# Kernel tuning notes

Measured on AMD Instinct MI355X. Metric: run time of the kernel, lower is better.

The kernel has to match this reference:

```python
import jax, jax.numpy as jnp
import numpy as np
import math

# Zero-indexed Fano plane lines: {i, i+1, i+3} mod 7
FANO_LINES = np.array([[0,1,3],[1,2,4],[2,3,5],[3,4,6],[4,5,0],[5,6,1],[6,0,2]])
WINDOW = 16  # local window hardcoded in create_expanded_mask

HIDDEN = 896
HEADS = 7
HEAD_DIM = HIDDEN // HEADS  # 128
B, T = 4, 2048


def fano_expanded_mask(T, causal):
    # line membership per head: [7, T] -> True where (j % 7) in line
    jm = np.arange(T) % 7
    line_hit = np.zeros((7, T), dtype=bool)
    for h in range(7):
        line_hit[h] = np.isin(jm, FANO_LINES[h])
    line_hit = jnp.asarray(line_hit)
    i = jnp.arange(T)[:, None]
    j = jnp.arange(T)[None, :]
    if causal:
        causal_m = j <= i                      # [T, T]
        local = (j >= i - WINDOW) & (j <= i)   # causal local window [i-16, i]
        mask = (line_hit[:, None, :] & causal_m[None]) | local[None]
    else:
        local = (j >= i - WINDOW) & (j <= i + WINDOW)
        mask = line_hit[:, None, :] | local[None]
    return mask  # [7, T, T], True = attend


def setup_inputs() -> dict:
    key = jax.random.key(0)
    kx, kq, kk, kv, ko = jax.random.split(key, 5)
    s = 1.0 / math.sqrt(HIDDEN)
    return {
        "x": jax.random.normal(kx, (B, T, HIDDEN), dtype=jnp.float32),
        "Wq": jax.random.normal(kq, (HEADS, HIDDEN, HEAD_DIM), dtype=jnp.float32) * s,
        "Wk": jax.random.normal(kk, (HEADS, HIDDEN, HEAD_DIM), dtype=jnp.float32) * s,
        "Wv": jax.random.normal(kv, (HEADS, HIDDEN, HEAD_DIM), dtype=jnp.float32) * s,
        "Wo": jax.random.normal(ko, (HIDDEN, HIDDEN), dtype=jnp.float32) * s,
        "is_causal": 1,
    }


def reference(x, Wq, Wk, Wv, Wo, is_causal):
    Bx, Tx, H = x.shape
    d = Wq.shape[-1]
    scale = 1.0 / math.sqrt(d)
    # per-head projections (no bias): [7, B, T, d]
    q = jnp.einsum('bth,nhd->nbtd', x, Wq)
    k = jnp.einsum('bth,nhd->nbtd', x, Wk)
    v = jnp.einsum('bth,nhd->nbtd', x, Wv)
    mask = fano_expanded_mask(Tx, bool(is_causal))        # [7, T, T]
    attn = jnp.einsum('nbtd,nbsd->nbts', q, k) * scale    # [7, B, T, T]
    attn = jnp.where(mask[:, None], attn, -jnp.inf)
    attn = jax.nn.softmax(attn, axis=-1)                  # every row has j=i valid
    out = jnp.einsum('nbts,nbsd->nbtd', attn, v)          # [7, B, T, d]
    combined = out.transpose(1, 2, 0, 3).reshape(Bx, Tx, H)  # concat heads
    return combined @ Wo.T
```

## Files before the change

### kernel.cpp

```cpp
#include <hip/hip_runtime.h>
#include <hip/hip_bf16.h>

#define HIDDEN 896
#define HEADS 7
#define HDIM 128
#define BB 4
#define TT 2048
#define MTOT (BB*TT)

#define SCP 896

typedef short bf16x8 __attribute__((ext_vector_type(8)));
typedef float f32x4 __attribute__((ext_vector_type(4)));

__device__ __forceinline__ short f2bf(float f) {
    union { float f; unsigned u; } v; v.f = f;
    unsigned r = (v.u + 0x7FFF + ((v.u >> 16) & 1)) >> 16;
    return (short)r;
}

__device__ __forceinline__ void gll16(const short* g, short* l) {
    __builtin_amdgcn_global_load_lds(
        (const __attribute__((address_space(1))) unsigned int*)g,
        (__attribute__((address_space(3))) unsigned int*)l, 16, 0, 0);
}

__device__ __forceinline__ unsigned linemask(int h) {
    return ((0x0Bu << h) | (0x0Bu >> (7 - h))) & 0x7Fu;
}
__device__ __forceinline__ int linecnt(unsigned m, int X) {
    return (X / 7) * 3 + __popc(m & ((1u << (X % 7)) - 1u));
}

#define NB_CASTX (MTOT * HIDDEN / 1024)
#define NB_CASTWO (HIDDEN * HIDDEN / 1024)
#define NB_TRANS (28 * 4 * 21)
__global__ __launch_bounds__(256) void prep_fused(
    const float* __restrict__ x, const float* __restrict__ Wo,
    const float* __restrict__ Wq, const float* __restrict__ Wk,
    const float* __restrict__ Wv,
    short* __restrict__ xb, short* __restrict__ Wob, short* __restrict__ Wt)
{
    __shared__ float tile[32][33];
    const int bid = blockIdx.x;
    if (bid < NB_CASTX) {
        int base = (bid * 256 + threadIdx.x) * 4;
        float4 v = *(const float4*)(x + base);
        short4 o;
        o.x = f2bf(v.x); o.y = f2bf(v.y); o.z = f2bf(v.z); o.w = f2bf(v.w);
        *(short4*)(xb + base) = o;
    } else if (bid < NB_CASTX + NB_CASTWO) {
        int base = ((bid - NB_CASTX) * 256 + threadIdx.x) * 4;
        float4 v = *(const float4*)(Wo + base);
        short4 o;
        o.x = f2bf(v.x); o.y = f2bf(v.y); o.z = f2bf(v.z); o.w = f2bf(v.w);
        *(short4*)(Wob + base) = o;
    } else {
        int t = bid - NB_CASTX - NB_CASTWO;
        const int z = t / 112;
        const int rem = t % 112;
        const int bx = rem % 28, by = rem / 28;
        const int type = z / 7, head = z % 7;
        const float* src = (type == 0 ? Wq : (type == 1 ? Wk : Wv)) + head * (HIDDEN * HDIM);
        short* dst = Wt + (size_t)z * (HDIM * HIDDEN);
        const int r0 = bx * 32, c0 = by * 32;
        const int tx = threadIdx.x & 31, ty = threadIdx.x >> 5;
        for (int i = 0; i < 4; i++)
            tile[ty * 4 + i][tx] = src[(r0 + ty * 4 + i) * HDIM + c0 + tx];
        __syncthreads();
        for (int i = 0; i < 4; i++)
            dst[(c0 + ty * 4 + i) * HIDDEN + r0 + tx] = f2bf(tile[tx][ty * 4 + i]);
    }
}

__global__ __launch_bounds__(256) void qkv_gemm(
    const short* __restrict__ xb, const short* __restrict__ Wt,
    short* __restrict__ Q, short* __restrict__ Kk, short* __restrict__ Vt)
{
    __shared__ short Ash[3 * 128 * 32];
    __shared__ short Bsh[3 * 128 * 32];
    const int orig = blockIdx.x;
    const int sblk = (orig & 7) * 168 + (orig >> 3);
    const int z = sblk % 21;
    const int m0 = (sblk / 21) * 128;
    const int head = z % 7, type = z / 7;
    const short* Wz = Wt + (size_t)z * (HDIM * HIDDEN);

    const int tid = threadIdx.x;
    const int wave = tid >> 6, lane = tid & 63;
    const int quad = lane >> 4, l16 = lane & 15;
    const int wm = (wave >> 1) * 64, wn = (wave & 1) * 64;

    f32x4 acc[4][4] = {};

    const int r0 = tid >> 2, cc0 = (tid & 3) * 8;
    const int r1 = r0 + 64;
    const short* asrc0 = xb + (size_t)(m0 + r0) * HIDDEN + cc0;
    const short* asrc1 = xb + (size_t)(m0 + r1) * HIDDEN + cc0;
    const short* bsrc0 = Wz + (size_t)r0 * HIDDEN + cc0;
    const short* bsrc1 = Wz + (size_t)r1 * HIDDEN + cc0;

    auto STAGE = [&](int kt, int sel) {
        const int ko = kt * 32;
        short* ab = Ash + sel * 4096;
        short* bb = Bsh + sel * 4096;
        gll16(asrc0 + ko, ab + wave * 512);
        gll16(asrc1 + ko, ab + 2048 + wave * 512);
        gll16(bsrc0 + ko, bb + wave * 512);
        gll16(bsrc1 + ko, bb + 2048 + wave * 512);
    };

    STAGE(0, 0);
    const int NT = HIDDEN / 32;
    for (int t = 0; t < NT; t++) {
        const int sel = t % 3;
        if (t + 1 < NT) {
            STAGE(t + 1, (t + 1) % 3);
            asm volatile("s_waitcnt vmcnt(4)" ::: "memory");
        } else {
            asm volatile("s_waitcnt vmcnt(0)" ::: "memory");
        }
        __builtin_amdgcn_s_barrier();
        __builtin_amdgcn_sched_barrier(0);
        const short* ab = Ash + sel * 4096;
        const short* bb = Bsh + sel * 4096;
        bf16x8 af[4], bfr[4];
        for (int mi = 0; mi < 4; mi++)
            af[mi] = *(const bf16x8*)(ab + (wm + mi * 16 + l16) * 32 + quad * 8);
        for (int ni = 0; ni < 4; ni++)
            bfr[ni] = *(const bf16x8*)(bb + (wn + ni * 16 + l16) * 32 + quad * 8);
        for (int mi = 0; mi < 4; mi++)
            for (int ni = 0; ni < 4; ni++)
                acc[mi][ni] = __builtin_amdgcn_mfma_f32_16x16x32_bf16(af[mi], bfr[ni], acc[mi][ni], 0, 0, 0);
    }

    const size_t base = (size_t)head * (MTOT * HDIM);
    if (type == 0) {
        const float qs = 0.08838834764831845f * 1.4426950408889634f;
        for (int mi = 0; mi < 4; mi++)
            for (int ni = 0; ni < 4; ni++)
                for (int r = 0; r < 4; r++) {
                    int m = m0 + wm + mi * 16 + quad * 4 + r;
                    int n = wn + ni * 16 + l16;
                    Q[base + (size_t)m * HDIM + n] = f2bf(acc[mi][ni][r] * qs);
                }
    } else if (type == 1) {
        for (int mi = 0; mi < 4; mi++)
            for (int ni = 0; ni < 4; ni++)
                for (int r = 0; r < 4; r++) {
                    int m = m0 + wm + mi * 16 + quad * 4 + r;
                    int n = wn + ni * 16 + l16;
                    Kk[base + (size_t)m * HDIM + n] = f2bf(acc[mi][ni][r]);
                }
    } else {
        for (int mi = 0; mi < 4; mi++)
            for (int ni = 0; ni < 4; ni++) {
                int m = m0 + wm + mi * 16 + quad * 4;
                int bb2 = m >> 11, t = m & 2047;
                int n = wn + ni * 16 + l16;
                short4 o;
                o.x = f2bf(acc[mi][ni][0]); o.y = f2bf(acc[mi][ni][1]);
                o.z = f2bf(acc[mi][ni][2]); o.w = f2bf(acc[mi][ni][3]);
                *(short4*)(Vt + base + (size_t)bb2 * (HDIM * TT) + (size_t)n * TT + t) = o;
            }
    }
}

__global__ __launch_bounds__(256) void compact_k(const short* __restrict__ K,
                                                 short* __restrict__ Kc)
{
    const int hb = blockIdx.x, h = hb >> 2, b = hb & 3;
    const unsigned m = linemask(h);
    const int c_tot = 876 + __popc(m & 0xFu);
    const int o0 = __ffs(m) - 1;
    const unsigned m1 = m & (m - 1);
    const int o1 = __ffs(m1) - 1;
    const unsigned m2 = m1 & (m1 - 1);
    const int o2 = __ffs(m2) - 1;
    const int r = blockIdx.y * 32 + (threadIdx.x >> 3);
    const int c = (threadIdx.x & 7) * 16;
    short* dst = Kc + ((size_t)hb * SCP + r) * HDIM + c;
    if (r < c_tot) {
        int g = r / 3, id = r - g * 3;
        int s = g * 7 + (id == 0 ? o0 : (id == 1 ? o1 : o2));
        const short* src = K + (size_t)(h * MTOT + b * TT + s) * HDIM + c;
        *(bf16x8*)dst = *(const bf16x8*)src;
        *(bf16x8*)(dst + 8) = *(const bf16x8*)(src + 8);
    } else {
        bf16x8 zz = {};
        *(bf16x8*)dst = zz;
        *(bf16x8*)(dst + 8) = zz;
    }
}

__global__ __launch_bounds__(256) void compact_v(const short* __restrict__ Vt,
                                                 short* __restrict__ Vc)
{
    const int hb = blockIdx.x, h = hb >> 2, b = hb & 3;
    const int d = blockIdx.y;
    const unsigned m = linemask(h);
    const int c_tot = 876 + __popc(m & 0xFu);
    const int o0 = __ffs(m) - 1;
    const unsigned m1 = m & (m - 1);
    const int o1 = __ffs(m1) - 1;
    const unsigned m2 = m1 & (m1 - 1);
    const int o2 = __ffs(m2) - 1;
    const short* src = Vt + (size_t)h * MTOT * HDIM + (size_t)b * HDIM * TT + (size_t)d * TT;
    short* dst = Vc + ((size_t)hb * HDIM + d) * SCP;
    for (int sp = threadIdx.x * 4; sp < SCP; sp += 1024) {
        short4 o;
        short* po = (short*)&o;
        for (int j = 0; j < 4; j++) {
            int spp = sp + j;
            short v = 0;
            if (spp < c_tot) {
                int g = spp / 3, id = spp - g * 3;
                int s = g * 7 + (id == 0 ? o0 : (id == 1 ? o1 : o2));
                v = src[s];
            }
            po[j] = v;
        }
        *(short4*)(dst + sp) = o;
    }
}

__global__ __launch_bounds__(256) void fano_attn(
    const short* __restrict__ Q, const short* __restrict__ K, const short* __restrict__ Vt,
    const short* __restrict__ Kc, const short* __restrict__ Vc,
    short* __restrict__ Ocat, const int* __restrict__ iscp)
{
    __shared__ short Ks[2 * 64 * 128];
    __shared__ short Vs[2 * 128 * 64];
    __shared__ short Ps[4 * 2048];

    const int causal = *iscp;
    const int mlin = blockIdx.y + 4 * blockIdx.z;
    const int qt = (causal && mlin >= 16) ? ((int)gridDim.x - 1 - blockIdx.x)
                                          : (int)blockIdx.x;
    const int q0 = qt * 128;
    const int b = blockIdx.y, h = blockIdx.z;
    const int hb = h * 4 + b;
    const int tid = threadIdx.x, wave = tid >> 6, lane = tid & 63;
    const int quad = lane >> 4, l16 = lane & 15;
    const int iw = q0 + wave * 32;
    const int swz = l16 & 7;

    const short* Qb = Q + (size_t)(h * MTOT + b * TT + q0) * HDIM;
    const short* Kb = K + (size_t)(h * MTOT + b * TT) * HDIM;
    const short* Vb = Vt + (size_t)h * MTOT * HDIM + (size_t)b * HDIM * TT;
    const short* Kcb = Kc + (size_t)hb * SCP * HDIM;
    const short* Vcb = Vc + (size_t)hb * HDIM * SCP;

    int krowS[4], kccS[4], vrowS[4], vccS[4];
    for (int i = 0; i < 4; i++) {
        int c = (wave * 4 + i) * 64 + lane;
        krowS[i] = c >> 4; kccS[i] = ((c & 15) ^ (krowS[i] & 7)) * 8;
        vrowS[i] = c >> 3; vccS[i] = ((c & 7) ^ (vrowS[i] & 7)) * 8;
    }

    auto STAGE = [&](const short* Kp, const short* Vp, int vstr, int s0, int sel) {
        short* kb = Ks + sel * 8192;
        short* vb = Vs + sel * 8192;
        for (int i = 0; i < 4; i++) {
            gll16(Kp + (size_t)(s0 + krowS[i]) * HDIM + kccS[i], kb + (wave * 4 + i) * 512);
            gll16(Vp + (size_t)vrowS[i] * vstr + s0 + vccS[i], vb + (wave * 4 + i) * 512);
        }
    };

    bf16x8 qf[2][4];
    for (int g = 0; g < 2; g++)
        for (int ks = 0; ks < 4; ks++)
            qf[g][ks] = *(const bf16x8*)(Qb + (size_t)(wave * 32 + g * 16 + l16) * HDIM + ks * 32 + quad * 8);

    f32x4 oacc[2][8] = {};
    f32x4 lacc[2] = {};
    int irow[2][4];
    for (int g = 0; g < 2; g++)
        for (int r = 0; r < 4; r++)
            irow[g][r] = q0 + wave * 32 + g * 16 + quad * 4 + r;

    const bf16x8 vones = {0x3F80, 0x3F80, 0x3F80, 0x3F80, 0x3F80, 0x3F80, 0x3F80, 0x3F80};

    const unsigned m_h = linemask(h);
    const int c_tot = 876 + __popc(m_h & 0xFu);
    const int sB0 = (causal && q0 >= 64) ? (q0 - 64) : 0;
    const int sB1 = causal ? (q0 + 128) : (q0 + 192 < TT ? q0 + 192 : TT);
    const int cA = linecnt(m_h, sB0);
    const int cC0 = causal ? c_tot : linecnt(m_h, sB1);
    const int l16h = (l16 - h + 7) % 7;

    const short* Kpa[3]; const short* Vpa[3];
    int vstra[3], ta0[3], ta1[3], cv0a[3], cv1a[3], cmpa[3];
    int np = 0;
    {
        int t1A = (cA + 63) >> 6;
        if (t1A > 0) { Kpa[np] = Kcb; Vpa[np] = Vcb; vstra[np] = SCP; ta0[np] = 0; ta1[np] = t1A; cv0a[np] = 0; cv1a[np] = cA; cmpa[np] = 1; np++; }
    }
    {
        int t0B = sB0 >> 6, t1B = sB1 >> 6;
        if (t1B > t0B) { Kpa[np] = Kb; Vpa[np] = Vb; vstra[np] = TT; ta0[np] = t0B; ta1[np] = t1B; cv0a[np] = 0; cv1a[np] = 0; cmpa[np] = 0; np++; }
    }
    if (!causal) {
        int t0C = cC0 >> 6, t1C = (c_tot + 63) >> 6;
        if (t1C > t0C) { Kpa[np] = Kcb; Vpa[np] = Vcb; vstra[np] = SCP; ta0[np] = t0C; ta1[np] = t1C; cv0a[np] = cC0; cv1a[np] = c_tot; cmpa[np] = 1; np++; }
    }

    short* Pw = Ps + wave * 2048;
    int cur = 0;
    STAGE(Kpa[0], Vpa[0], vstra[0], ta0[0] * 64, 0);

    for (int pi = 0; pi < np; pi++) {
        const short* Kp_ = Kpa[pi];
        const short* Vp_ = Vpa[pi];
        const int vstr_ = vstra[pi], t1_ = ta1[pi];
        const int comp = cmpa[pi], c0v = cv0a[pi], c1v = cv1a[pi];
        for (int t = ta0[pi]; t < t1_; t++) {
            asm volatile("s_waitcnt vmcnt(0)" ::: "memory");
            __builtin_amdgcn_s_barrier();
            __builtin_amdgcn_sched_barrier(0);
            if (t + 1 < t1_)
                STAGE(Kp_, Vp_, vstr_, (t + 1) * 64, cur ^ 1);
            else if (pi + 1 < np)
                STAGE(Kpa[pi + 1], Vpa[pi + 1], vstra[pi + 1], ta0[pi + 1] * 64, cur ^ 1);

            const short* KsC = Ks + cur * 8192;
            const short* VsC = Vs + cur * 8192;
            const int s0 = t * 64;

            f32x4 sacc[2][4] = {};
            for (int ni = 0; ni < 4; ni++)
                for (int ks = 0; ks < 4; ks++) {
                    bf16x8 bk = *(const bf16x8*)(KsC + (ni * 16 + l16) * 128 + ((ks * 4 + quad) ^ swz) * 8);
                    sacc[0][ni] = __builtin_amdgcn_mfma_f32_16x16x32_bf16(qf[0][ks], bk, sacc[0][ni], 0, 0, 0);
                    sacc[1][ni] = __builtin_amdgcn_mfma_f32_16x16x32_bf16(qf[1][ks], bk, sacc[1][ni], 0, 0, 0);
                }

            if (comp) {
                for (int ni = 0; ni < 4; ni++) {
                    int scol = s0 + ni * 16 + l16;
                    bool ok = (scol >= c0v) & (scol < c1v);
                    for (int g = 0; g < 2; g++)
                        for (int r = 0; r < 4; r++)
                            sacc[g][ni][r] = ok ? exp2f(sacc[g][ni][r]) : 0.0f;
                }
            } else {
                const bool full = (s0 + 80 > iw) && (causal || (s0 < iw + 48));
                int d7b = l16h + (t % 7); if (d7b >= 7) d7b -= 7;
                if (full) {
                    for (int ni = 0; ni < 4; ni++) {
                        int d7 = d7b + 2 * ni; if (d7 >= 7) d7 -= 7;
                        bool line = (0x0B >> d7) & 1;
                        int s = s0 + ni * 16 + l16;
                        for (int g = 0; g < 2; g++)
                            for (int r = 0; r < 4; r++) {
                                int i = irow[g][r];
                                bool ok = causal ? ((s <= i) & (line | (s >= i - 16)))
                                                 : (line | ((s >= i - 16) & (s <= i + 16)));
                                sacc[g][ni][r] = ok ? exp2f(sacc[g][ni][r]) : 0.0f;
                            }
                    }
                } else {
                    for (int ni = 0; ni < 4; ni++) {
                        int d7 = d7b + 2 * ni; if (d7 >= 7) d7 -= 7;
                        bool line = (0x0B >> d7) & 1;
                        for (int g = 0; g < 2; g++)
                            for (int r = 0; r < 4; r++)
                                sacc[g][ni][r] = line ? exp2f(sacc[g][ni][r]) : 0.0f;
                    }
                }
            }

            for (int g = 0; g < 2; g++)
                for (int ni = 0; ni < 4; ni++)
                    for (int r = 0; r < 4; r++) {
                        int row = g * 16 + quad * 4 + r;
                        Pw[row * 64 + (((ni * 2 + (l16 >> 3)) ^ (row & 7)) * 8) + (l16 & 7)]
                            = f2bf(sacc[g][ni][r]);
                    }

            for (int ks2 = 0; ks2 < 2; ks2++) {
                bf16x8 ap0 = *(const bf16x8*)(Pw + l16 * 64 + ((ks2 * 4 + quad) ^ swz) * 8);
                bf16x8 ap1 = *(const bf16x8*)(Pw + (16 + l16) * 64 + ((ks2 * 4 + quad) ^ swz) * 8);
                lacc[0] = __builtin_amdgcn_mfma_f32_16x16x32_bf16(ap0, vones, lacc[0], 0, 0, 0);
                lacc[1] = __builtin_amdgcn_mfma_f32_16x16x32_bf16(ap1, vones, lacc[1], 0, 0, 0);
                for (int nj = 0; nj < 8; nj++) {
                    bf16x8 bv = *(const bf16x8*)(VsC + (nj * 16 + l16) * 64 + ((ks2 * 4 + quad) ^ swz) * 8);
                    oacc[0][nj] = __builtin_amdgcn_mfma_f32_16x16x32_bf16(ap0, bv, oacc[0][nj], 0, 0, 0);
                    oacc[1][nj] = __builtin_amdgcn_mfma_f32_16x16x32_bf16(ap1, bv, oacc[1][nj], 0, 0, 0);
                }
            }
            cur ^= 1;
        }
    }

    short* Obase = Ocat + (size_t)(b * TT) * HIDDEN + h * HDIM;
    for (int g = 0; g < 2; g++) {
        float inv[4];
        for (int r = 0; r < 4; r++) inv[r] = 1.0f / lacc[g][r];
        for (int nj = 0; nj < 8; nj++)
            for (int r = 0; r < 4; r++)
                Obase[(size_t)irow[g][r] * HIDDEN + nj * 16 + l16] = f2bf(oacc[g][nj][r] * inv[r]);
    }
}

__global__ __launch_bounds__(256) void out_gemm(
    const short* __restrict__ A, const short* __restrict__ Bt, float* __restrict__ out)
{
    __shared__ short Ash[3 * 128 * 32];
    __shared__ short Bsh[3 * 128 * 32];
    const int orig = blockIdx.x;
    const int sblk = (orig & 7) * 56 + (orig >> 3);
    const int n0 = (sblk % 7) * 128;
    const int m0 = (sblk / 7) * 128;

    const int tid = threadIdx.x;
    const int wave = tid >> 6, lane = tid & 63;
    const int quad = lane >> 4, l16 = lane & 15;
    const int wm = (wave >> 1) * 64, wn = (wave & 1) * 64;

    f32x4 acc[4][4] = {};

    const int r0 = tid >> 2, cc0 = (tid & 3) * 8;
    const int r1 = r0 + 64;
    const short* asrc0 = A + (size_t)(m0 + r0) * HIDDEN + cc0;
    const short* asrc1 = A + (size_t)(m0 + r1) * HIDDEN + cc0;
    const short* bsrc0 = Bt + (size_t)(n0 + r0) * HIDDEN + cc0;
    const short* bsrc1 = Bt + (size_t)(n0 + r1) * HIDDEN + cc0;

    auto STAGE = [&](int kt, int sel) {
        const int ko = kt * 32;
        short* ab = Ash + sel * 4096;
        short* bb = Bsh + sel * 4096;
        gll16(asrc0 + ko, ab + wave * 512);
        gll16(asrc1 + ko, ab + 2048 + wave * 512);
        gll16(bsrc0 + ko, bb + wave * 512);
        gll16(bsrc1 + ko, bb + 2048 + wave * 512);
    };

    STAGE(0, 0);
    const int NT = HIDDEN / 32;
    for (int t = 0; t < NT; t++) {
        const int sel = t % 3;
        if (t + 1 < NT) {
            STAGE(t + 1, (t + 1) % 3);
            asm volatile("s_waitcnt vmcnt(4)" ::: "memory");
        } else {
            asm volatile("s_waitcnt vmcnt(0)" ::: "memory");
        }
        __builtin_amdgcn_s_barrier();
        __builtin_amdgcn_sched_barrier(0);
        const short* ab = Ash + sel * 4096;
        const short* bb = Bsh + sel * 4096;
        bf16x8 af[4], bfr[4];
        for (int mi = 0; mi < 4; mi++)
            af[mi] = *(const bf16x8*)(ab + (wm + mi * 16 + l16) * 32 + quad * 8);
        for (int ni = 0; ni < 4; ni++)
            bfr[ni] = *(const bf16x8*)(bb + (wn + ni * 16 + l16) * 32 + quad * 8);
        for (int mi = 0; mi < 4; mi++)
            for (int ni = 0; ni < 4; ni++)
                acc[mi][ni] = __builtin_amdgcn_mfma_f32_16x16x32_bf16(af[mi], bfr[ni], acc[mi][ni], 0, 0, 0);
    }

    for (int mi = 0; mi < 4; mi++)
        for (int ni = 0; ni < 4; ni++)
            for (int r = 0; r < 4; r++) {
                int m = m0 + wm + mi * 16 + quad * 4 + r;
                int n = n0 + wn + ni * 16 + l16;
                out[(size_t)m * HIDDEN + n] = acc[mi][ni][r];
            }
}

extern "C" void kernel_launch(void* const* d_in, const int* in_sizes, int n_in,
                              void* d_out, int out_size, void* d_ws, size_t ws_size,
                              hipStream_t stream) {
    (void)in_sizes; (void)n_in; (void)out_size; (void)ws_size;
    const float* x  = (const float*)d_in[0];
    const float* Wq = (const float*)d_in[1];
    const float* Wk = (const float*)d_in[2];
    const float* Wv = (const float*)d_in[3];
    const float* Wo = (const float*)d_in[4];
    const int* iscp = (const int*)d_in[5];
    float* out = (float*)d_out;

    short* xb   = (short*)d_ws;
    short* Qb   = xb   + (size_t)MTOT * HIDDEN;
    short* Kb   = Qb   + (size_t)HEADS * MTOT * HDIM;
    short* Vtb  = Kb   + (size_t)HEADS * MTOT * HDIM;
    short* Ocat = Vtb  + (size_t)HEADS * MTOT * HDIM;
    short* Wt   = Ocat;
    short* Wob  = Ocat + (size_t)MTOT * HIDDEN;
    short* Kc   = xb;
    short* Vc   = Kc + (size_t)28 * SCP * HDIM;

    prep_fused<<<NB_CASTX + NB_CASTWO + NB_TRANS, 256, 0, stream>>>(
        x, Wo, Wq, Wk, Wv, xb, Wob, Wt);
    qkv_gemm<<<21 * (MTOT / 128), 256, 0, stream>>>(xb, Wt, Qb, Kb, Vtb);
    compact_k<<<dim3(28, SCP / 32), 256, 0, stream>>>(Kb, Kc);
    compact_v<<<dim3(28, HDIM), 256, 0, stream>>>(Vtb, Vc);
    fano_attn<<<dim3(TT / 128, BB, HEADS), 256, 0, stream>>>(Qb, Kb, Vtb, Kc, Vc, Ocat, iscp);
    out_gemm<<<(HIDDEN / 128) * (MTOT / 128), 256, 0, stream>>>(Ocat, Wob, out);
}
```

Measured before the change: 279.6 us.

## Split attention KV steps across two wave groups with LDS reduction

Doubles the attention block to 512 threads, forming two groups of four waves that handle alternating key/value tiles for the same 128 query rows, each with its own double-buffered LDS staging. At the end, group 1 writes its partial output and row-sum accumulators to shared memory and group 0 adds them before normalizing and storing. The aim is to shorten each block's serial KV loop and raise wave-level parallelism on the 448-block grid. The cost is a larger LDS footprint (160 KB), fewer resident blocks per CU, an extra reduction pass, and a simplified causal tile ordering.

```diff
diff --git a/kernel.cpp b/kernel.cpp
--- a/kernel.cpp
+++ b/kernel.cpp
@@ -224,25 +224,22 @@
     }
 }
 
-__global__ __launch_bounds__(256) void fano_attn(
+__global__ __launch_bounds__(512) void fano_attn(
     const short* __restrict__ Q, const short* __restrict__ K, const short* __restrict__ Vt,
     const short* __restrict__ Kc, const short* __restrict__ Vc,
     short* __restrict__ Ocat, const int* __restrict__ iscp)
 {
-    __shared__ short Ks[2 * 64 * 128];
-    __shared__ short Vs[2 * 128 * 64];
-    __shared__ short Ps[4 * 2048];
+    __shared__ short L[81920];
 
     const int causal = *iscp;
-    const int mlin = blockIdx.y + 4 * blockIdx.z;
-    const int qt = (causal && mlin >= 16) ? ((int)gridDim.x - 1 - blockIdx.x)
-                                          : (int)blockIdx.x;
+    const int qt = causal ? (TT / 128 - 1 - (int)blockIdx.x) : (int)blockIdx.x;
     const int q0 = qt * 128;
     const int b = blockIdx.y, h = blockIdx.z;
     const int hb = h * 4 + b;
-    const int tid = threadIdx.x, wave = tid >> 6, lane = tid & 63;
+    const int tid = threadIdx.x;
+    const int wave = tid >> 6, grp = wave >> 2, wg = wave & 3, lane = tid & 63;
     const int quad = lane >> 4, l16 = lane & 15;
-    const int iw = q0 + wave * 32;
+    const int iw = q0 + wg * 32;
     const int swz = l16 & 7;
 
     const short* Qb = Q + (size_t)(h * MTOT + b * TT + q0) * HDIM;
@@ -253,31 +250,31 @@
 
     int krowS[4], kccS[4], vrowS[4], vccS[4];
     for (int i = 0; i < 4; i++) {
-        int c = (wave * 4 + i) * 64 + lane;
+        int c = (wg * 4 + i) * 64 + lane;
         krowS[i] = c >> 4; kccS[i] = ((c & 15) ^ (krowS[i] & 7)) * 8;
         vrowS[i] = c >> 3; vccS[i] = ((c & 7) ^ (vrowS[i] & 7)) * 8;
     }
 
-    auto STAGE = [&](const short* Kp, const short* Vp, int vstr, int s0, int sel) {
-        short* kb = Ks + sel * 8192;
-        short* vb = Vs + sel * 8192;
+    auto STAGE = [&](const short* Kp, const short* Vp, int vstr, int s0, int c) {
+        short* kb = L + (grp * 2 + c) * 16384;
+        short* vb = kb + 8192;
         for (int i = 0; i < 4; i++) {
-            gll16(Kp + (size_t)(s0 + krowS[i]) * HDIM + kccS[i], kb + (wave * 4 + i) * 512);
-            gll16(Vp + (size_t)vrowS[i] * vstr + s0 + vccS[i], vb + (wave * 4 + i) * 512);
+            gll16(Kp + (size_t)(s0 + krowS[i]) * HDIM + kccS[i], kb + (wg * 4 + i) * 512);
+            gll16(Vp + (size_t)vrowS[i] * vstr + s0 + vccS[i], vb + (wg * 4 + i) * 512);
         }
     };
 
     bf16x8 qf[2][4];
     for (int g = 0; g < 2; g++)
         for (int ks = 0; ks < 4; ks++)
-            qf[g][ks] = *(const bf16x8*)(Qb + (size_t)(wave * 32 + g * 16 + l16) * HDIM + ks * 32 + quad * 8);
+            qf[g][ks] = *(const bf16x8*)(Qb + (size_t)(wg * 32 + g * 16 + l16) * HDIM + ks * 32 + quad * 8);
 
     f32x4 oacc[2][8] = {};
     f32x4 lacc[2] = {};
     int irow[2][4];
     for (int g = 0; g < 2; g++)
         for (int r = 0; r < 4; r++)
-            irow[g][r] = q0 + wave * 32 + g * 16 + quad * 4 + r;
+            irow[g][r] = q0 + wg * 32 + g * 16 + quad * 4 + r;
 
     const bf16x8 vones = {0x3F80, 0x3F80, 0x3F80, 0x3F80, 0x3F80, 0x3F80, 0x3F80, 0x3F80};
 
@@ -304,27 +301,44 @@
         int t0C = cC0 >> 6, t1C = (c_tot + 63) >> 6;
         if (t1C > t0C) { Kpa[np] = Kcb; Vpa[np] = Vcb; vstra[np] = SCP; ta0[np] = t0C; ta1[np] = t1C; cv0a[np] = cC0; cv1a[np] = c_tot; cmpa[np] = 1; np++; }
     }
-
-    short* Pw = Ps + wave * 2048;
+    int ns = 0;
+    for (int i = 0; i < np; i++) ns += ta1[i] - ta0[i];
+
+    auto stepOf = [&](int u, int& pi, int& t) {
+        int acc = 0;
+        for (int i = 0; i < np; i++) {
+            int len = ta1[i] - ta0[i];
+            if (u < acc + len) { pi = i; t = ta0[i] + (u - acc); return; }
+            acc += len;
+        }
+        pi = 0; t = ta0[0];
+    };
+
+    short* Pw = L + 65536 + wave * 2048;
     int cur = 0;
-    STAGE(Kpa[0], Vpa[0], vstra[0], ta0[0] * 64, 0);
-
-    for (int pi = 0; pi < np; pi++) {
-        const short* Kp_ = Kpa[pi];
-        const short* Vp_ = Vpa[pi];
-        const int vstr_ = vstra[pi], t1_ = ta1[pi];
-        const int comp = cmpa[pi], c0v = cv0a[pi], c1v = cv1a[pi];
-        for (int t = ta0[pi]; t < t1_; t++) {
-            asm volatile("s_waitcnt vmcnt(0)" ::: "memory");
-            __builtin_amdgcn_s_barrier();
-            __builtin_amdgcn_sched_barrier(0);
-            if (t + 1 < t1_)
-                STAGE(Kp_, Vp_, vstr_, (t + 1) * 64, cur ^ 1);
-            else if (pi + 1 < np)
-                STAGE(Kpa[pi + 1], Vpa[pi + 1], vstra[pi + 1], ta0[pi + 1] * 64, cur ^ 1);
-
-            const short* KsC = Ks + cur * 8192;
-            const short* VsC = Vs + cur * 8192;
+
+    {
+        int pi, t; stepOf(grp, pi, t);
+        STAGE(Kpa[pi], Vpa[pi], vstra[pi], t * 64, 0);
+    }
+
+    const int nrounds = (ns + 1) >> 1;
+    for (int j = 0; j < nrounds; j++) {
+        const int u = 2 * j + grp;
+        const bool act = (u < ns);
+        if (act) asm volatile("s_waitcnt vmcnt(0)" ::: "memory");
+        __builtin_amdgcn_s_barrier();
+        __builtin_amdgcn_sched_barrier(0);
+        const int un = u + 2;
+        if (un < ns) {
+            int pn, tn; stepOf(un, pn, tn);
+            STAGE(Kpa[pn], Vpa[pn], vstra[pn], tn * 64, cur ^ 1);
+        }
+        if (act) {
+            int pi, t; stepOf(u, pi, t);
+            const int comp = cmpa[pi], c0v = cv0a[pi], c1v = cv1a[pi];
+            const short* KsC = L + (grp * 2 + cur) * 16384;
+            const short* VsC = KsC + 8192;
             const int s0 = t * 64;
 
             f32x4 sacc[2][4] = {};
@@ -389,17 +403,38 @@
                     oacc[1][nj] = __builtin_amdgcn_mfma_f32_16x16x32_bf16(ap1, bv, oacc[1][nj], 0, 0, 0);
                 }
             }
-            cur ^= 1;
-        }
-    }
-
-    short* Obase = Ocat + (size_t)(b * TT) * HIDDEN + h * HDIM;
-    for (int g = 0; g < 2; g++) {
-        float inv[4];
-        for (int r = 0; r < 4; r++) inv[r] = 1.0f / lacc[g][r];
-        for (int nj = 0; nj < 8; nj++)
-            for (int r = 0; r < 4; r++)
-                Obase[(size_t)irow[g][r] * HIDDEN + nj * 16 + l16] = f2bf(oacc[g][nj][r] * inv[r]);
+        }
+        cur ^= 1;
+    }
+
+    __syncthreads();
+    float* Lf = (float*)L;
+    if (grp == 1) {
+        float* od = Lf + wg * 4096;
+        for (int g = 0; g < 2; g++)
+            for (int nj = 0; nj < 8; nj++)
+                *(f32x4*)(od + ((g * 8 + nj) * 64 + lane) * 4) = oacc[g][nj];
+        float* ld = Lf + 16384 + wg * 512;
+        for (int g = 0; g < 2; g++)
+            *(f32x4*)(ld + (g * 64 + lane) * 4) = lacc[g];
+    }
+    __syncthreads();
+    if (grp == 0) {
+        float* od = Lf + wg * 4096;
+        float* ld = Lf + 16384 + wg * 512;
+        for (int g = 0; g < 2; g++) {
+            lacc[g] += *(const f32x4*)(ld + (g * 64 + lane) * 4);
+            for (int nj = 0; nj < 8; nj++)
+                oacc[g][nj] += *(const f32x4*)(od + ((g * 8 + nj) * 64 + lane) * 4);
+        }
+        short* Obase = Ocat + (size_t)(b * TT) * HIDDEN + h * HDIM;
+        for (int g = 0; g < 2; g++) {
+            float inv[4];
+            for (int r = 0; r < 4; r++) inv[r] = 1.0f / lacc[g][r];
+            for (int nj = 0; nj < 8; nj++)
+                for (int r = 0; r < 4; r++)
+                    Obase[(size_t)irow[g][r] * HIDDEN + nj * 16 + l16] = f2bf(oacc[g][nj][r] * inv[r]);
+        }
     }
 }
 
@@ -497,6 +532,6 @@
     qkv_gemm<<<21 * (MTOT / 128), 256, 0, stream>>>(xb, Wt, Qb, Kb, Vtb);
     compact_k<<<dim3(28, SCP / 32), 256, 0, stream>>>(Kb, Kc);
     compact_v<<<dim3(28, HDIM), 256, 0, stream>>>(Vtb, Vc);
-    fano_attn<<<dim3(TT / 128, BB, HEADS), 256, 0, stream>>>(Qb, Kb, Vtb, Kc, Vc, Ocat, iscp);
+    fano_attn<<<dim3(TT / 128, BB, HEADS), 512, 0, stream>>>(Qb, Kb, Vtb, Kc, Vc, Ocat, iscp);
     out_gemm<<<(HIDDEN / 128) * (MTOT / 128), 256, 0, stream>>>(Ocat, Wob, out);
 }
```

Result: faster. 273.0 us (-2.4%).
